# Kernel tuning notes

Measured on AMD Instinct MI355X. Metric: run time of the kernel, lower is better.

The kernel has to match this reference:

```python
import jax, jax.numpy as jnp
import numpy as np

N_NODES = 100000
N_EDGES = 819200
D = 512
L = 3
LN_EPS = 1e-5


def setup_inputs() -> dict:
    key = jax.random.key(0)
    ks = jax.random.split(key, 8)
    x = jax.random.normal(ks[0], (N_NODES, D), dtype=jnp.float32)
    edge_index = jax.random.randint(ks[1], (2, N_EDGES), 0, N_NODES, dtype=jnp.int32)
    scale = 1.0 / np.sqrt(D)
    W_l = jax.random.normal(ks[2], (L, D, D), dtype=jnp.float32) * scale  # neighbor transform
    W_r = jax.random.normal(ks[3], (L, D, D), dtype=jnp.float32) * scale  # root transform
    b = jax.random.normal(ks[4], (L, D), dtype=jnp.float32) * 0.01
    ln_g = jnp.ones((L, D), dtype=jnp.float32)
    ln_b = jnp.zeros((L, D), dtype=jnp.float32)
    return {"x": x, "edge_index": edge_index, "W_l": W_l, "W_r": W_r,
            "b": b, "ln_g": ln_g, "ln_b": ln_b}


def reference(x, edge_index, W_l, W_r, b, ln_g, ln_b):
    # SAGEConv (mean aggr) x L layers, each followed by LayerNorm, ReLU,
    # dropout (p=0, identity in eval) and residual add. batch=None -> node embeddings.
    src = edge_index[0]  # message sources (x_j)
    tgt = edge_index[1]  # aggregation targets (x_i)
    n = x.shape[0]
    cnt = jax.ops.segment_sum(jnp.ones((src.shape[0],), x.dtype), tgt, num_segments=n)
    inv_cnt = (1.0 / jnp.maximum(cnt, 1.0))[:, None]  # mean; isolated nodes -> 0
    for i in range(W_l.shape[0]):
        x_in = x
        agg = jax.ops.segment_sum(x[src], tgt, num_segments=n) * inv_cnt  # [N, D]
        h = agg @ W_l[i].T + x @ W_r[i].T + b[i]
        mu = jnp.mean(h, axis=-1, keepdims=True)
        var = jnp.mean(jnp.square(h - mu), axis=-1, keepdims=True)
        h = (h - mu) * jax.lax.rsqrt(var + LN_EPS) * ln_g[i] + ln_b[i]
        h = jax.nn.relu(h)
        x = h + x_in  # residual (shapes always match: D==D)
    return x
```

## Files before the change

kernel.cpp:

```cpp
#include <hip/hip_runtime.h>
#include <hip/hip_bf16.h>
#include <cstdint>

#define N_NODES 100000
#define N_EDGES 819200
#define D 512
#define LAYERS 3
#define LN_EPS 1e-5f

#define GEMM_GRID 782

typedef __bf16 bf16x8 __attribute__((ext_vector_type(8)));
typedef float floatx4 __attribute__((ext_vector_type(4)));

__device__ __forceinline__ void bf2x2(uint32_t u, float& lo, float& hi) {
    union { uint32_t i; float f; } a, b;
    a.i = u << 16; b.i = u & 0xFFFF0000u;
    lo = a.f; hi = b.f;
}
__device__ __forceinline__ uint16_t f2bf(float f) {
    union { float f; uint32_t i; } v; v.f = f;
    uint32_t r = v.i + 0x7FFFu + ((v.i >> 16) & 1u);
    return (uint16_t)(r >> 16);
}
__device__ __forceinline__ uint32_t f2bf2(float lo, float hi) {
    return (uint32_t)f2bf(lo) | ((uint32_t)f2bf(hi) << 16);
}

__device__ __forceinline__ void async16(const uint16_t* g, uint16_t* lds) {
    __builtin_amdgcn_global_load_lds(
        (const __attribute__((address_space(1))) uint32_t*)g,
        (__attribute__((address_space(3))) uint32_t*)lds, 16, 0, 0);
}

#define BARRIER() do { asm volatile("" ::: "memory"); \
                       __builtin_amdgcn_s_barrier();   \
                       asm volatile("" ::: "memory"); } while (0)
#define VMCNT6() asm volatile("s_waitcnt vmcnt(6)" ::: "memory")
#define VMCNT0() asm volatile("s_waitcnt vmcnt(0)" ::: "memory")

__global__ void k_count(const int* __restrict__ tgt, int* __restrict__ cnt) {
    int e = blockIdx.x * blockDim.x + threadIdx.x;
    if (e < N_EDGES) atomicAdd(&cnt[tgt[e]], 1);
}

__global__ void k_scan(const int* __restrict__ cnt, int* __restrict__ row_start,
                       int* __restrict__ cursor) {
    __shared__ int wsum[16];
    const int t = threadIdx.x;
    const int lane = t & 63, wid = t >> 6;
    int running = 0;
    for (int base = 0; base < N_NODES; base += 1024) {
        int idx = base + t;
        int v = (idx < N_NODES) ? cnt[idx] : 0;
        int x = v;
        #pragma unroll
        for (int off = 1; off < 64; off <<= 1) {
            int n = __shfl_up(x, off, 64);
            if (lane >= off) x += n;
        }
        if (lane == 63) wsum[wid] = x;
        __syncthreads();
        if (wid == 0) {
            int s = (lane < 16) ? wsum[lane] : 0;
            #pragma unroll
            for (int off = 1; off < 16; off <<= 1) {
                int n = __shfl_up(s, off, 64);
                if (lane >= off) s += n;
            }
            if (lane < 16) wsum[lane] = s;
        }
        __syncthreads();
        int waveoff = (wid > 0) ? wsum[wid - 1] : 0;
        int excl = running + x + waveoff - v;
        if (idx < N_NODES) { row_start[idx] = excl; cursor[idx] = excl; }
        int chunk_total = wsum[15];
        __syncthreads();
        running += chunk_total;
    }
    if (t == 0) row_start[N_NODES] = running;
}

__global__ void k_scatter(const int* __restrict__ src, const int* __restrict__ tgt,
                          int* __restrict__ cursor, int* __restrict__ src_sorted) {
    int e = blockIdx.x * blockDim.x + threadIdx.x;
    if (e < N_EDGES) {
        int p = atomicAdd(&cursor[tgt[e]], 1);
        src_sorted[p] = src[e];
    }
}

__global__ void k_f2bf(const float* __restrict__ in, uint16_t* __restrict__ out, int n) {
    int i = (blockIdx.x * blockDim.x + threadIdx.x) * 8;
    if (i < n) {
        float4 a = *(const float4*)(in + i);
        float4 b = *(const float4*)(in + i + 4);
        uint4 o;
        o.x = f2bf2(a.x, a.y); o.y = f2bf2(a.z, a.w);
        o.z = f2bf2(b.x, b.y); o.w = f2bf2(b.z, b.w);
        *(uint4*)(out + i) = o;
    }
}

__global__ void k_wcat(const float* __restrict__ Wl, const float* __restrict__ Wr,
                       uint16_t* __restrict__ wcat) {
    int i = blockIdx.x * blockDim.x + threadIdx.x;
    int k = i & 1023;
    int j = (i >> 10) & 511;
    int l = i >> 19;
    float v = (k < 512) ? Wl[((size_t)l * 512 + j) * 512 + k]
                        : Wr[((size_t)l * 512 + j) * 512 + (k - 512)];
    wcat[i] = f2bf(v);
}

__device__ __forceinline__ void agg_acc(float* acc, uint4 p) {
    float lo, hi;
    bf2x2(p.x, lo, hi); acc[0] += lo; acc[1] += hi;
    bf2x2(p.y, lo, hi); acc[2] += lo; acc[3] += hi;
    bf2x2(p.z, lo, hi); acc[4] += lo; acc[5] += hi;
    bf2x2(p.w, lo, hi); acc[6] += lo; acc[7] += hi;
}

__global__ __launch_bounds__(256)
void k_agg(const uint16_t* __restrict__ x_bf, const int* __restrict__ row_start,
           const int* __restrict__ src_sorted, uint16_t* __restrict__ agg_bf) {
    const int wid = threadIdx.x >> 6, lane = threadIdx.x & 63;
    const int node = blockIdx.x * 4 + wid;
    if (node >= N_NODES) return;
    const int s0 = row_start[node], s1 = row_start[node + 1];
    const int col = lane * 8;
    float acc[8] = {0.f, 0.f, 0.f, 0.f, 0.f, 0.f, 0.f, 0.f};
    int e = s0;
    for (; e + 4 <= s1; e += 4) {
        int i0 = src_sorted[e], i1 = src_sorted[e + 1];
        int i2 = src_sorted[e + 2], i3 = src_sorted[e + 3];
        uint4 p0 = *(const uint4*)(x_bf + (size_t)i0 * D + col);
        uint4 p1 = *(const uint4*)(x_bf + (size_t)i1 * D + col);
        uint4 p2 = *(const uint4*)(x_bf + (size_t)i2 * D + col);
        uint4 p3 = *(const uint4*)(x_bf + (size_t)i3 * D + col);
        agg_acc(acc, p0); agg_acc(acc, p1); agg_acc(acc, p2); agg_acc(acc, p3);
    }
    if (e + 2 <= s1) {
        int i0 = src_sorted[e], i1 = src_sorted[e + 1];
        uint4 p0 = *(const uint4*)(x_bf + (size_t)i0 * D + col);
        uint4 p1 = *(const uint4*)(x_bf + (size_t)i1 * D + col);
        agg_acc(acc, p0); agg_acc(acc, p1);
        e += 2;
    }
    if (e < s1) {
        int i0 = src_sorted[e];
        uint4 p0 = *(const uint4*)(x_bf + (size_t)i0 * D + col);
        agg_acc(acc, p0);
    }
    const float inv = (s1 > s0) ? 1.0f / (float)(s1 - s0) : 0.0f;
    uint4 o;
    o.x = f2bf2(acc[0] * inv, acc[1] * inv);
    o.y = f2bf2(acc[2] * inv, acc[3] * inv);
    o.z = f2bf2(acc[4] * inv, acc[5] * inv);
    o.w = f2bf2(acc[6] * inv, acc[7] * inv);
    *(uint4*)(agg_bf + (size_t)node * D + col) = o;
}

__global__ __launch_bounds__(512, 1)
void k_gemm(const uint16_t* __restrict__ A0,
            const uint16_t* __restrict__ A1,
            const uint16_t* __restrict__ W,
            uint16_t* __restrict__ Hout)
{
    __shared__ uint16_t Ash0[256 * 64];
    __shared__ uint16_t Ash1[256 * 64];
    __shared__ uint16_t Bsh0[256 * 64];
    __shared__ uint16_t Bsh1[256 * 64];

    const int tid = threadIdx.x;
    const int l = tid & 63, w = tid >> 6;
    const int wm = w >> 2, wn = w & 3;
    const int wmA = wm * 128, wnB = wn * 64;
    const int mrow = l & 15, qbase = l >> 4, sw7 = l & 7;

    const int bid = blockIdx.x;
    const int xcd = bid & 7, pos = bid >> 3;
    const int wk = (xcd < 6 ? xcd * 98 : 588 + (xcd - 6) * 97) + pos;
    const int rb = wk >> 1, cb = wk & 1;
    const int row0 = rb * 256, col0 = cb * 256;

    const int ra = w * 8 + (l >> 3);
    const int o16 = (l & 7) ^ ((l >> 3) & 7);
    uint32_t offA[2][2], offB[2][2];
    #pragma unroll
    for (int h = 0; h < 2; h++)
        #pragma unroll
        for (int j = 0; j < 2; j++) {
            int rr = h * 128 + j * 64 + ra;
            int gra = row0 + rr; if (gra > N_NODES - 1) gra = N_NODES - 1;
            offA[h][j] = (uint32_t)gra * 1024u + (uint32_t)o16 * 16u;
            offB[h][j] = (uint32_t)(col0 + rr) * 2048u + (uint32_t)o16 * 16u;
        }

    auto stA = [&](uint16_t* buf, int h, int t_) {
        int ts = t_ < 15 ? t_ : 15;
        const char* base; uint32_t koff;
        if (ts < 8) { base = (const char*)A0; koff = (uint32_t)ts * 128u; }
        else        { base = (const char*)A1; koff = (uint32_t)(ts - 8) * 128u; }
        async16((const uint16_t*)(base + offA[h][0] + koff), buf + (h * 128 + w * 8) * 64);
        async16((const uint16_t*)(base + offA[h][1] + koff), buf + (h * 128 + 64 + w * 8) * 64);
    };
    auto stB = [&](uint16_t* buf, int h, int t_) {
        int ts = t_ < 15 ? t_ : 15;
        uint32_t koff = (uint32_t)ts * 128u;
        async16((const uint16_t*)((const char*)W + offB[h][0] + koff), buf + (h * 128 + w * 8) * 64);
        async16((const uint16_t*)((const char*)W + offB[h][1] + koff), buf + (h * 128 + 64 + w * 8) * 64);
    };

    floatx4 acc[8][4] = {};
    bf16x8 af[4][2], bA[2][2], bB[2][2];

    auto rdA4 = [&](bf16x8 a_[4][2], const uint16_t* buf, int rbase) {
        #pragma unroll
        for (int mr = 0; mr < 4; mr++) {
            int r = wmA + rbase + mr * 16 + mrow;
            #pragma unroll
            for (int kh = 0; kh < 2; kh++) {
                int slot = (kh * 4 + qbase) ^ sw7;
                a_[mr][kh] = *(const bf16x8*)(buf + r * 64 + slot * 8);
            }
        }
    };
    auto rdB2 = [&](bf16x8 b_[2][2], const uint16_t* buf, int nbase) {
        #pragma unroll
        for (int nr = 0; nr < 2; nr++) {
            int r = wnB + (nbase + nr) * 16 + mrow;
            #pragma unroll
            for (int kh = 0; kh < 2; kh++) {
                int slot = (kh * 4 + qbase) ^ sw7;
                b_[nr][kh] = *(const bf16x8*)(buf + r * 64 + slot * 8);
            }
        }
    };
    auto quad = [&](const bf16x8 a_[4][2], const bf16x8 b_[2][2], int mb, int nb) {
        __builtin_amdgcn_s_setprio(1);
        #pragma unroll
        for (int mr = 0; mr < 4; mr++)
            #pragma unroll
            for (int nr = 0; nr < 2; nr++)
                #pragma unroll
                for (int kh = 0; kh < 2; kh++)
                    acc[mb + mr][nb + nr] = __builtin_amdgcn_mfma_f32_16x16x32_bf16(
                        a_[mr][kh], b_[nr][kh], acc[mb + mr][nb + nr], 0, 0, 0);
        __builtin_amdgcn_s_setprio(0);
    };

    stB(Bsh0, 0, 0); stB(Bsh0, 1, 0); stA(Ash0, 0, 0); stA(Ash0, 1, 0);
    stB(Bsh1, 0, 1); stB(Bsh1, 1, 1); stA(Ash1, 0, 1);
    VMCNT6();
    BARRIER();

    #pragma unroll 1
    for (int i = 0; i < 8; i++) {
        const int te = 2 * i, to = 2 * i + 1;
        rdA4(af, Ash0, 0); rdB2(bA, Bsh0, 0);
        stA(Ash1, 1, to);
        BARRIER(); quad(af, bA, 0, 0); BARRIER();
        rdB2(bB, Bsh0, 2);
        BARRIER(); quad(af, bB, 0, 2); BARRIER();
        rdA4(af, Ash0, 64);
        stB(Bsh0, 0, te + 2); stB(Bsh0, 1, te + 2);
        BARRIER(); quad(af, bA, 4, 0); BARRIER();
        stA(Ash0, 0, te + 2);
        VMCNT6();
        BARRIER(); quad(af, bB, 4, 2); BARRIER();
        rdA4(af, Ash1, 0); rdB2(bA, Bsh1, 0);
        stA(Ash0, 1, te + 2);
        BARRIER(); quad(af, bA, 0, 0); BARRIER();
        rdB2(bB, Bsh1, 2);
        BARRIER(); quad(af, bB, 0, 2); BARRIER();
        rdA4(af, Ash1, 64);
        stB(Bsh1, 0, to + 2); stB(Bsh1, 1, to + 2);
        BARRIER(); quad(af, bA, 4, 0); BARRIER();
        stA(Ash1, 0, to + 2);
        VMCNT6();
        BARRIER(); quad(af, bB, 4, 2); BARRIER();
    }
    VMCNT0();

    #pragma unroll
    for (int mr = 0; mr < 8; mr++) {
        #pragma unroll
        for (int rr = 0; rr < 4; rr++) {
            int grow = row0 + wmA + mr * 16 + qbase * 4 + rr;
            if (grow < N_NODES) {
                #pragma unroll
                for (int nr = 0; nr < 4; nr++) {
                    int gcol = col0 + wnB + nr * 16 + mrow;
                    Hout[(size_t)grow * 512 + gcol] = f2bf(acc[mr][nr][rr]);
                }
            }
        }
    }
}

__global__ __launch_bounds__(256)
void k_ln(const uint16_t* __restrict__ H, const float* __restrict__ bias,
          const float* __restrict__ gam, const float* __restrict__ bet,
          uint16_t* __restrict__ xbf,
          float* __restrict__ out32, int last) {
    const int wid = threadIdx.x >> 6, lane = threadIdx.x & 63;
    const int node = blockIdx.x * 4 + wid;
    if (node >= N_NODES) return;
    const int col = lane * 8;
    const size_t off = (size_t)node * D + col;

    uint4 hp = *(const uint4*)(H + off);
    float v[8];
    bf2x2(hp.x, v[0], v[1]); bf2x2(hp.y, v[2], v[3]);
    bf2x2(hp.z, v[4], v[5]); bf2x2(hp.w, v[6], v[7]);
    float4 b0 = *(const float4*)(bias + col), b1 = *(const float4*)(bias + col + 4);
    v[0] += b0.x; v[1] += b0.y; v[2] += b0.z; v[3] += b0.w;
    v[4] += b1.x; v[5] += b1.y; v[6] += b1.z; v[7] += b1.w;

    float s = 0.f;
    #pragma unroll
    for (int i = 0; i < 8; i++) s += v[i];
    #pragma unroll
    for (int o = 32; o >= 1; o >>= 1) s += __shfl_xor(s, o, 64);
    float mu = s * (1.0f / D);
    float vs = 0.f;
    #pragma unroll
    for (int i = 0; i < 8; i++) { float d = v[i] - mu; vs += d * d; }
    #pragma unroll
    for (int o = 32; o >= 1; o >>= 1) vs += __shfl_xor(vs, o, 64);
    float rstd = rsqrtf(vs * (1.0f / D) + LN_EPS);

    float4 g0 = *(const float4*)(gam + col), g1 = *(const float4*)(gam + col + 4);
    float4 e0 = *(const float4*)(bet + col), e1 = *(const float4*)(bet + col + 4);
    float gg[8] = {g0.x, g0.y, g0.z, g0.w, g1.x, g1.y, g1.z, g1.w};
    float ee[8] = {e0.x, e0.y, e0.z, e0.w, e1.x, e1.y, e1.z, e1.w};

    uint4 xp = *(const uint4*)(xbf + off);
    float xi[8];
    bf2x2(xp.x, xi[0], xi[1]); bf2x2(xp.y, xi[2], xi[3]);
    bf2x2(xp.z, xi[4], xi[5]); bf2x2(xp.w, xi[6], xi[7]);

    float o_[8];
    #pragma unroll
    for (int i = 0; i < 8; i++) {
        float h = (v[i] - mu) * rstd * gg[i] + ee[i];
        o_[i] = fmaxf(h, 0.f) + xi[i];
    }
    if (last) {
        float4 f0 = {o_[0], o_[1], o_[2], o_[3]};
        float4 f1 = {o_[4], o_[5], o_[6], o_[7]};
        *(float4*)(out32 + off) = f0;
        *(float4*)(out32 + off + 4) = f1;
    } else {
        uint4 o;
        o.x = f2bf2(o_[0], o_[1]); o.y = f2bf2(o_[2], o_[3]);
        o.z = f2bf2(o_[4], o_[5]); o.w = f2bf2(o_[6], o_[7]);
        *(uint4*)(xbf + off) = o;
    }
}

extern "C" void kernel_launch(void* const* d_in, const int* in_sizes, int n_in,
                              void* d_out, int out_size, void* d_ws, size_t ws_size,
                              hipStream_t stream) {
    const float* x   = (const float*)d_in[0];
    const int*   ei  = (const int*)d_in[1];
    const float* Wl  = (const float*)d_in[2];
    const float* Wr  = (const float*)d_in[3];
    const float* b   = (const float*)d_in[4];
    const float* g   = (const float*)d_in[5];
    const float* be  = (const float*)d_in[6];
    float* out = (float*)d_out;
    const int* src = ei;
    const int* tgt = ei + N_EDGES;

    size_t off = 0;
    auto alloc = [&](size_t bytes) -> void* {
        void* p = (char*)d_ws + off;
        off += (bytes + 255) & ~(size_t)255;
        return p;
    };
    int* cnt        = (int*)alloc((size_t)N_NODES * 4);
    int* row_start  = (int*)alloc((size_t)(N_NODES + 1) * 4);
    int* cursor     = (int*)alloc((size_t)N_NODES * 4);
    int* src_sorted = (int*)alloc((size_t)N_EDGES * 4);
    uint16_t* wcat  = (uint16_t*)alloc((size_t)LAYERS * 512 * 1024 * 2);
    uint16_t* x_bf  = (uint16_t*)alloc((size_t)N_NODES * D * 2);
    uint16_t* agg_bf= (uint16_t*)alloc((size_t)N_NODES * D * 2);
    uint16_t* h_bf  = (uint16_t*)alloc((size_t)N_NODES * D * 2);

    (void)hipMemsetAsync(cnt, 0, (size_t)N_NODES * 4, stream);
    k_count<<<N_EDGES / 256, 256, 0, stream>>>(tgt, cnt);
    k_scan<<<1, 1024, 0, stream>>>(cnt, row_start, cursor);
    k_scatter<<<N_EDGES / 256, 256, 0, stream>>>(src, tgt, cursor, src_sorted);
    k_f2bf<<<(N_NODES * D / 8) / 256, 256, 0, stream>>>(x, x_bf, N_NODES * D);
    k_wcat<<<(LAYERS * 512 * 1024) / 256, 256, 0, stream>>>(Wl, Wr, wcat);

    for (int l = 0; l < LAYERS; l++) {
        k_agg<<<N_NODES / 4, 256, 0, stream>>>(x_bf, row_start, src_sorted, agg_bf);
        k_gemm<<<GEMM_GRID, 512, 0, stream>>>(agg_bf, x_bf,
                                              wcat + (size_t)l * 512 * 1024, h_bf);
        k_ln<<<N_NODES / 4, 256, 0, stream>>>(h_bf, b + l * D, g + l * D, be + l * D,
                                              x_bf, out, l == 2 ? 1 : 0);
    }
}
```

Baseline: 1.490 ms.

## Fuse LayerNorm epilogue into GEMM via per-row-tile completion counter

Removes the separate LayerNorm kernel. Each GEMM block bumps an atomic counter for its 256-row tile, and whichever of the two column blocks finishes second runs bias, LayerNorm, ReLU and residual for those rows. It reads H back from global memory, which is likely still in cache. This is meant to cut a launch per layer and overlap the LayerNorm work with the GEMM tail. The cost is that one block handles 256 rows serially, 32 per wave, so the LayerNorm part may be latency-bound. It also relies on threadfence ordering between the two blocks.

```diff
diff --git a/kernel.cpp b/kernel.cpp
--- a/kernel.cpp
+++ b/kernel.cpp
@@ -9,6 +9,7 @@
 #define LN_EPS 1e-5f
 
 #define GEMM_GRID 782
+#define ROW_TILES 391
 
 typedef __bf16 bf16x8 __attribute__((ext_vector_type(8)));
 typedef float floatx4 __attribute__((ext_vector_type(4)));
@@ -163,14 +164,20 @@
 
 __global__ __launch_bounds__(512, 1)
 void k_gemm(const uint16_t* __restrict__ A0,
-            const uint16_t* __restrict__ A1,
+            uint16_t* __restrict__ xbf,
             const uint16_t* __restrict__ W,
-            uint16_t* __restrict__ Hout)
+            uint16_t* __restrict__ Hout,
+            const float* __restrict__ bias,
+            const float* __restrict__ gam,
+            const float* __restrict__ bet,
+            int* __restrict__ tick,
+            float* __restrict__ out32, int last)
 {
     __shared__ uint16_t Ash0[256 * 64];
     __shared__ uint16_t Ash1[256 * 64];
     __shared__ uint16_t Bsh0[256 * 64];
     __shared__ uint16_t Bsh1[256 * 64];
+    __shared__ int s_old;
 
     const int tid = threadIdx.x;
     const int l = tid & 63, w = tid >> 6;
@@ -201,7 +208,7 @@
         int ts = t_ < 15 ? t_ : 15;
         const char* base; uint32_t koff;
         if (ts < 8) { base = (const char*)A0; koff = (uint32_t)ts * 128u; }
-        else        { base = (const char*)A1; koff = (uint32_t)(ts - 8) * 128u; }
+        else        { base = (const char*)xbf; koff = (uint32_t)(ts - 8) * 128u; }
         async16((const uint16_t*)(base + offA[h][0] + koff), buf + (h * 128 + w * 8) * 64);
         async16((const uint16_t*)(base + offA[h][1] + koff), buf + (h * 128 + 64 + w * 8) * 64);
     };
@@ -297,66 +304,67 @@
             }
         }
     }
-}
-
-__global__ __launch_bounds__(256)
-void k_ln(const uint16_t* __restrict__ H, const float* __restrict__ bias,
-          const float* __restrict__ gam, const float* __restrict__ bet,
-          uint16_t* __restrict__ xbf,
-          float* __restrict__ out32, int last) {
-    const int wid = threadIdx.x >> 6, lane = threadIdx.x & 63;
-    const int node = blockIdx.x * 4 + wid;
-    if (node >= N_NODES) return;
-    const int col = lane * 8;
-    const size_t off = (size_t)node * D + col;
-
-    uint4 hp = *(const uint4*)(H + off);
-    float v[8];
-    bf2x2(hp.x, v[0], v[1]); bf2x2(hp.y, v[2], v[3]);
-    bf2x2(hp.z, v[4], v[5]); bf2x2(hp.w, v[6], v[7]);
-    float4 b0 = *(const float4*)(bias + col), b1 = *(const float4*)(bias + col + 4);
-    v[0] += b0.x; v[1] += b0.y; v[2] += b0.z; v[3] += b0.w;
-    v[4] += b1.x; v[5] += b1.y; v[6] += b1.z; v[7] += b1.w;
-
-    float s = 0.f;
-    #pragma unroll
-    for (int i = 0; i < 8; i++) s += v[i];
-    #pragma unroll
-    for (int o = 32; o >= 1; o >>= 1) s += __shfl_xor(s, o, 64);
-    float mu = s * (1.0f / D);
-    float vs = 0.f;
-    #pragma unroll
-    for (int i = 0; i < 8; i++) { float d = v[i] - mu; vs += d * d; }
-    #pragma unroll
-    for (int o = 32; o >= 1; o >>= 1) vs += __shfl_xor(vs, o, 64);
-    float rstd = rsqrtf(vs * (1.0f / D) + LN_EPS);
-
-    float4 g0 = *(const float4*)(gam + col), g1 = *(const float4*)(gam + col + 4);
-    float4 e0 = *(const float4*)(bet + col), e1 = *(const float4*)(bet + col + 4);
-    float gg[8] = {g0.x, g0.y, g0.z, g0.w, g1.x, g1.y, g1.z, g1.w};
-    float ee[8] = {e0.x, e0.y, e0.z, e0.w, e1.x, e1.y, e1.z, e1.w};
-
-    uint4 xp = *(const uint4*)(xbf + off);
-    float xi[8];
-    bf2x2(xp.x, xi[0], xi[1]); bf2x2(xp.y, xi[2], xi[3]);
-    bf2x2(xp.z, xi[4], xi[5]); bf2x2(xp.w, xi[6], xi[7]);
-
-    float o_[8];
-    #pragma unroll
-    for (int i = 0; i < 8; i++) {
-        float h = (v[i] - mu) * rstd * gg[i] + ee[i];
-        o_[i] = fmaxf(h, 0.f) + xi[i];
-    }
-    if (last) {
-        float4 f0 = {o_[0], o_[1], o_[2], o_[3]};
-        float4 f1 = {o_[4], o_[5], o_[6], o_[7]};
-        *(float4*)(out32 + off) = f0;
-        *(float4*)(out32 + off + 4) = f1;
-    } else {
-        uint4 o;
-        o.x = f2bf2(o_[0], o_[1]); o.y = f2bf2(o_[2], o_[3]);
-        o.z = f2bf2(o_[4], o_[5]); o.w = f2bf2(o_[6], o_[7]);
-        *(uint4*)(xbf + off) = o;
+
+    __threadfence();
+    if (tid == 0) s_old = atomicAdd(&tick[rb], 1);
+    __syncthreads();
+    if (s_old != 1) return;
+    __threadfence();
+
+    for (int rr8 = 0; rr8 < 32; rr8++) {
+        const int node = row0 + w * 32 + rr8;
+        if (node >= N_NODES) break;
+        const int col = l * 8;
+        const size_t off = (size_t)node * D + col;
+
+        uint4 hp = *(const uint4*)(Hout + off);
+        float v[8];
+        bf2x2(hp.x, v[0], v[1]); bf2x2(hp.y, v[2], v[3]);
+        bf2x2(hp.z, v[4], v[5]); bf2x2(hp.w, v[6], v[7]);
+        float4 b0 = *(const float4*)(bias + col), b1 = *(const float4*)(bias + col + 4);
+        v[0] += b0.x; v[1] += b0.y; v[2] += b0.z; v[3] += b0.w;
+        v[4] += b1.x; v[5] += b1.y; v[6] += b1.z; v[7] += b1.w;
+
+        float s = 0.f;
+        #pragma unroll
+        for (int i = 0; i < 8; i++) s += v[i];
+        #pragma unroll
+        for (int o = 32; o >= 1; o >>= 1) s += __shfl_xor(s, o, 64);
+        float mu = s * (1.0f / D);
+        float vs = 0.f;
+        #pragma unroll
+        for (int i = 0; i < 8; i++) { float d = v[i] - mu; vs += d * d; }
+        #pragma unroll
+        for (int o = 32; o >= 1; o >>= 1) vs += __shfl_xor(vs, o, 64);
+        float rstd = rsqrtf(vs * (1.0f / D) + LN_EPS);
+
+        float4 g0 = *(const float4*)(gam + col), g1 = *(const float4*)(gam + col + 4);
+        float4 e0 = *(const float4*)(bet + col), e1 = *(const float4*)(bet + col + 4);
+        float gg[8] = {g0.x, g0.y, g0.z, g0.w, g1.x, g1.y, g1.z, g1.w};
+        float ee[8] = {e0.x, e0.y, e0.z, e0.w, e1.x, e1.y, e1.z, e1.w};
+
+        uint4 xp = *(const uint4*)(xbf + off);
+        float xi[8];
+        bf2x2(xp.x, xi[0], xi[1]); bf2x2(xp.y, xi[2], xi[3]);
+        bf2x2(xp.z, xi[4], xi[5]); bf2x2(xp.w, xi[6], xi[7]);
+
+        float o_[8];
+        #pragma unroll
+        for (int i = 0; i < 8; i++) {
+            float h = (v[i] - mu) * rstd * gg[i] + ee[i];
+            o_[i] = fmaxf(h, 0.f) + xi[i];
+        }
+        if (last) {
+            float4 f0 = {o_[0], o_[1], o_[2], o_[3]};
+            float4 f1 = {o_[4], o_[5], o_[6], o_[7]};
+            *(float4*)(out32 + off) = f0;
+            *(float4*)(out32 + off + 4) = f1;
+        } else {
+            uint4 o;
+            o.x = f2bf2(o_[0], o_[1]); o.y = f2bf2(o_[2], o_[3]);
+            o.z = f2bf2(o_[4], o_[5]); o.w = f2bf2(o_[6], o_[7]);
+            *(uint4*)(xbf + off) = o;
+        }
     }
 }
 
@@ -384,12 +392,14 @@
     int* row_start  = (int*)alloc((size_t)(N_NODES + 1) * 4);
     int* cursor     = (int*)alloc((size_t)N_NODES * 4);
     int* src_sorted = (int*)alloc((size_t)N_EDGES * 4);
+    int* tick       = (int*)alloc((size_t)LAYERS * ROW_TILES * 4);
     uint16_t* wcat  = (uint16_t*)alloc((size_t)LAYERS * 512 * 1024 * 2);
     uint16_t* x_bf  = (uint16_t*)alloc((size_t)N_NODES * D * 2);
     uint16_t* agg_bf= (uint16_t*)alloc((size_t)N_NODES * D * 2);
     uint16_t* h_bf  = (uint16_t*)alloc((size_t)N_NODES * D * 2);
 
     (void)hipMemsetAsync(cnt, 0, (size_t)N_NODES * 4, stream);
+    (void)hipMemsetAsync(tick, 0, (size_t)LAYERS * ROW_TILES * 4, stream);
     k_count<<<N_EDGES / 256, 256, 0, stream>>>(tgt, cnt);
     k_scan<<<1, 1024, 0, stream>>>(cnt, row_start, cursor);
     k_scatter<<<N_EDGES / 256, 256, 0, stream>>>(src, tgt, cursor, src_sorted);
@@ -399,8 +409,8 @@
     for (int l = 0; l < LAYERS; l++) {
         k_agg<<<N_NODES / 4, 256, 0, stream>>>(x_bf, row_start, src_sorted, agg_bf);
         k_gemm<<<GEMM_GRID, 512, 0, stream>>>(agg_bf, x_bf,
-                                              wcat + (size_t)l * 512 * 1024, h_bf);
-        k_ln<<<N_NODES / 4, 256, 0, stream>>>(h_bf, b + l * D, g + l * D, be + l * D,
-                                              x_bf, out, l == 2 ? 1 : 0);
-    }
-}
+                                              wcat + (size_t)l * 512 * 1024, h_bf,
+                                              b + l * D, g + l * D, be + l * D,
+                                              tick + l * ROW_TILES, out, l == 2 ? 1 : 0);
+    }
+}
```

After: 2.739 ms. 1.84x slower.
